# Performance work log

Hardware: AMD Instinct MI355X
Metric: run time of the kernel (lower is better)

## Reference

```python
import jax, jax.numpy as jnp
import numpy as np

PATCH = (4, 4, 4)
EMBED_DIM = 768
MASK_RATIO = 0.75
LN_EPS = 1e-3  # keras LayerNormalization default epsilon


def _sin_pos_enc_3d(nH, nW, nD, embed_dim):
    # Mirrors SinPosEncoding3D: per-axis sin/cos interleaved, concat, truncate.
    channels = int(np.ceil(embed_dim / 6) * 2)
    if channels % 2:
        channels += 1
    inv_freq = jnp.asarray(
        1.0 / np.power(10000, np.arange(0, channels, 2) / np.float32(channels)),
        dtype=jnp.float32)

    def emb1(n):
        s = jnp.arange(n, dtype=jnp.float32)[:, None] * inv_freq[None, :]  # [n, channels//2]
        return jnp.stack([jnp.sin(s), jnp.cos(s)], axis=-1).reshape(n, channels)

    ex = jnp.broadcast_to(emb1(nH)[:, None, None, :], (nH, nW, nD, channels))
    ey = jnp.broadcast_to(emb1(nW)[None, :, None, :], (nH, nW, nD, channels))
    ez = jnp.broadcast_to(emb1(nD)[None, None, :, :], (nH, nW, nD, channels))
    emb = jnp.concatenate([ex, ey, ez], axis=-1)[..., :embed_dim]
    return emb.reshape(1, nH * nW * nD, embed_dim)  # [1, token_num, E]


def setup_inputs() -> dict:
    key = jax.random.key(0)
    k1, k2, k3, k4 = jax.random.split(key, 4)
    B, H, W, D, C = 4, 96, 96, 96, 1
    nH, nW, nD = H // PATCH[0], W // PATCH[1], D // PATCH[2]
    token_num = nH * nW * nD
    mask_num = int(token_num * MASK_RATIO)
    patch_dim = PATCH[0] * PATCH[1] * PATCH[2] * C
    return {
        "x": jax.random.normal(k1, (B, H, W, D, C), dtype=jnp.float32),
        "proj_w": jax.random.normal(k2, (patch_dim, EMBED_DIM), dtype=jnp.float32) * 0.02,
        "proj_b": jnp.zeros((EMBED_DIM,), dtype=jnp.float32),
        "mask_token": jax.random.normal(k3, (1, mask_num, patch_dim), dtype=jnp.float32),
        "gamma": jnp.ones((EMBED_DIM,), dtype=jnp.float32),
        "beta": jnp.zeros((EMBED_DIM,), dtype=jnp.float32),
        "perm": jax.random.permutation(k4, token_num).astype(jnp.int32),
    }


def reference(x, proj_w, proj_b, mask_token, gamma, beta, perm):
    B, H, W, D, C = x.shape
    p0, p1, p2 = PATCH
    nH, nW, nD = H // p0, W // p1, D // p2
    token_num = nH * nW * nD
    mask_num = int(token_num * MASK_RATIO)

    # im2col-style 3D patch extraction (matches tf.extract_volume_patches layout)
    patches = x.reshape(B, nH, p0, nW, p1, nD, p2, C)
    patches = patches.transpose(0, 1, 3, 5, 2, 4, 6, 7)
    patches_flat = patches.reshape(B, token_num, p0 * p1 * p2 * C)

    mask_idx = perm[:mask_num]
    unmask_idx = perm[mask_num:]

    penc = _sin_pos_enc_3d(nH, nW, nD, EMBED_DIM)  # [1, token_num, E]

    # unmasked tokens: gather -> dense proj -> pos-enc add
    unmask_tokens = jnp.take(patches_flat, unmask_idx, axis=1)       # [B, U, pdim]
    a = jnp.einsum('bup,pe->bue', unmask_tokens, proj_w) + proj_b \
        + jnp.take(penc, unmask_idx, axis=1)                          # [B, U, E]

    # masked tokens: learned mask token -> proj -> pos-enc add, broadcast over B
    b = jnp.einsum('omp,pe->ome', mask_token, proj_w) + proj_b \
        + jnp.take(penc, mask_idx, axis=1)                            # [1, M, E]
    b = jnp.broadcast_to(b, (B, mask_num, EMBED_DIM))

    out = jnp.concatenate([a, b], axis=1).reshape(B, nH, nW, nD, EMBED_DIM)

    # LayerNorm over last axis (keras default: eps=1e-3)
    mean = jnp.mean(out, axis=-1, keepdims=True)
    var = jnp.var(out, axis=-1, keepdims=True)
    out = (out - mean) * jax.lax.rsqrt(var + LN_EPS) * gamma + beta
    return out, mask_idx
```

## Files before the change

kernel.cpp:

```cpp
#include <hip/hip_runtime.h>
#include <math.h>

#define NTHREADS 256
#define TROWS 16
#define TOKN 13824
#define MASKN 10368
#define UNMASKN 3456
#define EMB 768
#define NPOS 24
#define NBATCH 4
#define ABLOCKS (TOKN / TROWS)
#define BBLOCKS (MASKN / TROWS)
#define TABN (NPOS * 256)

__global__ __launch_bounds__(NTHREADS) void setup_kernel(
    const int* __restrict__ perm, float* __restrict__ tabg,
    float* __restrict__ out_idx)
{
  int i = blockIdx.x * NTHREADS + threadIdx.x;
  if (i < MASKN) out_idx[i] = (float)perm[i];
  if (i < TABN) {
    const float c0 = 13.287712379549449f / 128.0f;
    int pos = i >> 8, e = i & 255, j = e >> 1;
    float s = (float)pos * exp2f(-(float)j * c0);
    tabg[i] = (e & 1) ? cosf(s) : sinf(s);
  }
}

__global__ __launch_bounds__(NTHREADS) void fused_embed_ln(
    const float* __restrict__ x, const float* __restrict__ W,
    const float* __restrict__ pb, const float* __restrict__ mt,
    const float* __restrict__ gmm, const float* __restrict__ bta,
    const int* __restrict__ perm, const float* __restrict__ tabg,
    float* __restrict__ out)
{
  __shared__ __align__(16) float patch[TROWS * 64];
  __shared__ float wred[TROWS][4][2];
  __shared__ float rowstat[TROWS][2];
  __shared__ int h256[TROWS], w256[TROWS], d256[TROWS];

  const int tid = threadIdx.x;
  const int blk = blockIdx.x;
  const bool isA = blk < ABLOCKS;

  if (tid < TROWS) {
    int r;
    if (isA) {
      int row0 = blk * TROWS;
      int u = row0 % UNMASKN + tid;
      r = perm[MASKN + u];
    } else {
      int m0 = (blk - ABLOCKS) * TROWS;
      r = perm[m0 + tid];
    }
    int h = r / 576; int rem = r - h * 576;
    int w = rem / 24; int d = rem - w * 24;
    h256[tid] = h << 8; w256[tid] = w << 8; d256[tid] = d << 8;
  }
  __syncthreads();

  if (isA) {
    int b = (blk * TROWS) / UNMASKN;
    int t = tid >> 4, seg = tid & 15;
    int h = h256[t] >> 8, w = w256[t] >> 8, d = d256[t] >> 8;
    int ph = seg >> 2, pw = seg & 3;
    const float4* src = (const float4*)(x +
        ((((long)b * 96 + h * 4 + ph) * 96 + (w * 4 + pw)) * 96 + d * 4));
    ((float4*)patch)[tid] = *src;
  } else {
    int m0 = (blk - ABLOCKS) * TROWS;
    const float4* src = (const float4*)(mt + (long)m0 * 64);
    ((float4*)patch)[tid] = src[tid];
  }
  __syncthreads();

  float a0[TROWS], a1[TROWS], a2[TROWS];
  #pragma unroll
  for (int t = 0; t < TROWS; ++t) { a0[t] = 0.f; a1[t] = 0.f; a2[t] = 0.f; }

  for (int k4 = 0; k4 < 16; ++k4) {
    const float* wp = W + k4 * 4 * EMB + tid;
    float w00 = wp[0],       w01 = wp[256],         w02 = wp[512];
    float w10 = wp[EMB],     w11 = wp[EMB + 256],   w12 = wp[EMB + 512];
    float w20 = wp[2*EMB],   w21 = wp[2*EMB + 256], w22 = wp[2*EMB + 512];
    float w30 = wp[3*EMB],   w31 = wp[3*EMB + 256], w32 = wp[3*EMB + 512];
    #pragma unroll
    for (int t = 0; t < TROWS; ++t) {
      float4 p = *((const float4*)(patch + t * 64 + k4 * 4));
      a0[t] += p.x * w00; a1[t] += p.x * w01; a2[t] += p.x * w02;
      a0[t] += p.y * w10; a1[t] += p.y * w11; a2[t] += p.y * w12;
      a0[t] += p.z * w20; a1[t] += p.z * w21; a2[t] += p.z * w22;
      a0[t] += p.w * w30; a1[t] += p.w * w31; a2[t] += p.w * w32;
    }
  }

  const float pb0 = pb[tid], pb1 = pb[tid + 256], pb2 = pb[tid + 512];
  const float g0 = gmm[tid], g1 = gmm[tid + 256], g2 = gmm[tid + 512];
  const float b0 = bta[tid], b1 = bta[tid + 256], b2 = bta[tid + 512];
  const int wv = tid >> 6, ln = tid & 63;

  #pragma unroll
  for (int t = 0; t < TROWS; ++t) {
    float v0 = a0[t] + pb0 + tabg[h256[t] + tid];
    float v1 = a1[t] + pb1 + tabg[w256[t] + tid];
    float v2 = a2[t] + pb2 + tabg[d256[t] + tid];
    a0[t] = v0; a1[t] = v1; a2[t] = v2;
    float s = v0 + v1 + v2;
    float q = v0 * v0 + v1 * v1 + v2 * v2;
    #pragma unroll
    for (int off = 32; off > 0; off >>= 1) {
      s += __shfl_down(s, off, 64);
      q += __shfl_down(q, off, 64);
    }
    if (ln == 0) { wred[t][wv][0] = s; wred[t][wv][1] = q; }
  }
  __syncthreads();
  if (tid < TROWS) {
    float s = wred[tid][0][0] + wred[tid][1][0] + wred[tid][2][0] + wred[tid][3][0];
    float q = wred[tid][0][1] + wred[tid][1][1] + wred[tid][2][1] + wred[tid][3][1];
    float mean = s * (1.0f / 768.0f);
    float var = q * (1.0f / 768.0f) - mean * mean;
    rowstat[tid][0] = mean;
    rowstat[tid][1] = 1.0f / sqrtf(var + 0.001f);
  }
  __syncthreads();

  if (isA) {
    int row0 = blk * TROWS;
    int b = row0 / UNMASKN;
    int u0 = row0 % UNMASKN;
    float* base = out + ((long)b * TOKN + u0) * EMB + tid;
    #pragma unroll
    for (int t = 0; t < TROWS; ++t) {
      float mean = rowstat[t][0], rstd = rowstat[t][1];
      float* o = base + (long)t * EMB;
      o[0]   = (a0[t] - mean) * rstd * g0 + b0;
      o[256] = (a1[t] - mean) * rstd * g1 + b1;
      o[512] = (a2[t] - mean) * rstd * g2 + b2;
    }
  } else {
    int m0 = (blk - ABLOCKS) * TROWS;
    float* base = out + ((long)UNMASKN + m0) * EMB + tid;
    #pragma unroll
    for (int t = 0; t < TROWS; ++t) {
      float mean = rowstat[t][0], rstd = rowstat[t][1];
      float o0 = (a0[t] - mean) * rstd * g0 + b0;
      float o1 = (a1[t] - mean) * rstd * g1 + b1;
      float o2 = (a2[t] - mean) * rstd * g2 + b2;
      float* o = base + (long)t * EMB;
      #pragma unroll
      for (int bb = 0; bb < NBATCH; ++bb) {
        o[0] = o0; o[256] = o1; o[512] = o2;
        o += (long)TOKN * EMB;
      }
    }
  }
}

extern "C" void kernel_launch(void* const* d_in, const int* in_sizes, int n_in,
                              void* d_out, int out_size, void* d_ws, size_t ws_size,
                              hipStream_t stream) {
  const float* x    = (const float*)d_in[0];
  const float* W    = (const float*)d_in[1];
  const float* pb   = (const float*)d_in[2];
  const float* mt   = (const float*)d_in[3];
  const float* gmm  = (const float*)d_in[4];
  const float* bta  = (const float*)d_in[5];
  const int*   perm = (const int*)d_in[6];
  float* out = (float*)d_out;
  float* out_idx = out + (long)NBATCH * TOKN * EMB;
  float* tabg = (float*)d_ws;

  setup_kernel<<<(MASKN + NTHREADS - 1) / NTHREADS, NTHREADS, 0, stream>>>(
      perm, tabg, out_idx);
  fused_embed_ln<<<ABLOCKS + BBLOCKS, NTHREADS, 0, stream>>>(
      x, W, pb, mt, gmm, bta, perm, tabg, out);
}
```

Baseline: 250.0 us.

## Use bf16 MFMA for patch projection with pre-transposed bf16 weights

The fp32 FMA patch-projection loop is replaced with bf16 MFMA 16x16x32 instructions. Patches are converted to bf16 in LDS, and the setup kernel now also transposes and converts the projection weights into a bf16 workspace buffer. The LayerNorm reduction and output layout are reworked to match the MFMA accumulator layout. This lowers the compute cost of the GEMM, but bf16 inputs reduce accuracy, and the output stores now write 16-wide column chunks per row instead of full contiguous rows.

```diff
diff --git a/kernel.cpp b/kernel.cpp
--- a/kernel.cpp
+++ b/kernel.cpp
@@ -12,9 +12,20 @@
 #define ABLOCKS (TOKN / TROWS)
 #define BBLOCKS (MASKN / TROWS)
 #define TABN (NPOS * 256)
+#define WN (64 * EMB)
+
+typedef __attribute__((ext_vector_type(8))) short short8;
+typedef __attribute__((ext_vector_type(4))) float f32x4;
+
+__device__ __forceinline__ short f2bf(float f) {
+  union { float f; unsigned u; } c; c.f = f;
+  unsigned u = c.u + 0x7FFFu + ((c.u >> 16) & 1u);
+  return (short)(u >> 16);
+}
 
 __global__ __launch_bounds__(NTHREADS) void setup_kernel(
-    const int* __restrict__ perm, float* __restrict__ tabg,
+    const float* __restrict__ W, const int* __restrict__ perm,
+    float* __restrict__ tabg, short* __restrict__ wsW,
     float* __restrict__ out_idx)
 {
   int i = blockIdx.x * NTHREADS + threadIdx.x;
@@ -25,19 +36,23 @@
     float s = (float)pos * exp2f(-(float)j * c0);
     tabg[i] = (e & 1) ? cosf(s) : sinf(s);
   }
-}
-
-__global__ __launch_bounds__(NTHREADS) void fused_embed_ln(
-    const float* __restrict__ x, const float* __restrict__ W,
-    const float* __restrict__ pb, const float* __restrict__ mt,
-    const float* __restrict__ gmm, const float* __restrict__ bta,
-    const int* __restrict__ perm, const float* __restrict__ tabg,
+  if (i < WN) {
+    int col = i >> 6, k = i & 63;
+    wsW[i] = f2bf(W[k * EMB + col]);
+  }
+}
+
+__global__ __launch_bounds__(NTHREADS) void fused_embed_ln_mfma(
+    const float* __restrict__ x, const float* __restrict__ pb,
+    const float* __restrict__ mt, const float* __restrict__ gmm,
+    const float* __restrict__ bta, const int* __restrict__ perm,
+    const float* __restrict__ tabg, const short* __restrict__ wsW,
     float* __restrict__ out)
 {
-  __shared__ __align__(16) float patch[TROWS * 64];
+  __shared__ __align__(16) short aLds[TROWS][72];
+  __shared__ int segbase[3][TROWS];
   __shared__ float wred[TROWS][4][2];
   __shared__ float rowstat[TROWS][2];
-  __shared__ int h256[TROWS], w256[TROWS], d256[TROWS];
 
   const int tid = threadIdx.x;
   const int blk = blockIdx.x;
@@ -46,112 +61,127 @@
   if (tid < TROWS) {
     int r;
     if (isA) {
-      int row0 = blk * TROWS;
-      int u = row0 % UNMASKN + tid;
+      int u = (blk * TROWS) % UNMASKN + tid;
       r = perm[MASKN + u];
     } else {
-      int m0 = (blk - ABLOCKS) * TROWS;
-      r = perm[m0 + tid];
+      r = perm[(blk - ABLOCKS) * TROWS + tid];
     }
     int h = r / 576; int rem = r - h * 576;
     int w = rem / 24; int d = rem - w * 24;
-    h256[tid] = h << 8; w256[tid] = w << 8; d256[tid] = d << 8;
-  }
-  __syncthreads();
-
-  if (isA) {
-    int b = (blk * TROWS) / UNMASKN;
+    segbase[0][tid] = h << 8; segbase[1][tid] = w << 8; segbase[2][tid] = d << 8;
+  }
+  __syncthreads();
+
+  {
     int t = tid >> 4, seg = tid & 15;
-    int h = h256[t] >> 8, w = w256[t] >> 8, d = d256[t] >> 8;
-    int ph = seg >> 2, pw = seg & 3;
-    const float4* src = (const float4*)(x +
-        ((((long)b * 96 + h * 4 + ph) * 96 + (w * 4 + pw)) * 96 + d * 4));
-    ((float4*)patch)[tid] = *src;
-  } else {
-    int m0 = (blk - ABLOCKS) * TROWS;
-    const float4* src = (const float4*)(mt + (long)m0 * 64);
-    ((float4*)patch)[tid] = src[tid];
-  }
-  __syncthreads();
-
-  float a0[TROWS], a1[TROWS], a2[TROWS];
-  #pragma unroll
-  for (int t = 0; t < TROWS; ++t) { a0[t] = 0.f; a1[t] = 0.f; a2[t] = 0.f; }
-
-  for (int k4 = 0; k4 < 16; ++k4) {
-    const float* wp = W + k4 * 4 * EMB + tid;
-    float w00 = wp[0],       w01 = wp[256],         w02 = wp[512];
-    float w10 = wp[EMB],     w11 = wp[EMB + 256],   w12 = wp[EMB + 512];
-    float w20 = wp[2*EMB],   w21 = wp[2*EMB + 256], w22 = wp[2*EMB + 512];
-    float w30 = wp[3*EMB],   w31 = wp[3*EMB + 256], w32 = wp[3*EMB + 512];
-    #pragma unroll
-    for (int t = 0; t < TROWS; ++t) {
-      float4 p = *((const float4*)(patch + t * 64 + k4 * 4));
-      a0[t] += p.x * w00; a1[t] += p.x * w01; a2[t] += p.x * w02;
-      a0[t] += p.y * w10; a1[t] += p.y * w11; a2[t] += p.y * w12;
-      a0[t] += p.z * w20; a1[t] += p.z * w21; a2[t] += p.z * w22;
-      a0[t] += p.w * w30; a1[t] += p.w * w31; a2[t] += p.w * w32;
-    }
-  }
-
-  const float pb0 = pb[tid], pb1 = pb[tid + 256], pb2 = pb[tid + 512];
-  const float g0 = gmm[tid], g1 = gmm[tid + 256], g2 = gmm[tid + 512];
-  const float b0 = bta[tid], b1 = bta[tid + 256], b2 = bta[tid + 512];
-  const int wv = tid >> 6, ln = tid & 63;
-
-  #pragma unroll
-  for (int t = 0; t < TROWS; ++t) {
-    float v0 = a0[t] + pb0 + tabg[h256[t] + tid];
-    float v1 = a1[t] + pb1 + tabg[w256[t] + tid];
-    float v2 = a2[t] + pb2 + tabg[d256[t] + tid];
-    a0[t] = v0; a1[t] = v1; a2[t] = v2;
-    float s = v0 + v1 + v2;
-    float q = v0 * v0 + v1 * v1 + v2 * v2;
-    #pragma unroll
-    for (int off = 32; off > 0; off >>= 1) {
-      s += __shfl_down(s, off, 64);
-      q += __shfl_down(q, off, 64);
-    }
-    if (ln == 0) { wred[t][wv][0] = s; wred[t][wv][1] = q; }
+    float4 v;
+    if (isA) {
+      int b = (blk * TROWS) / UNMASKN;
+      int h = segbase[0][t] >> 8, w = segbase[1][t] >> 8, d = segbase[2][t] >> 8;
+      int ph = seg >> 2, pw = seg & 3;
+      v = *(const float4*)(x +
+          ((((long)b * 96 + h * 4 + ph) * 96 + (w * 4 + pw)) * 96 + d * 4));
+    } else {
+      int m0 = (blk - ABLOCKS) * TROWS;
+      v = *(const float4*)(mt + (long)(m0 + t) * 64 + seg * 4);
+    }
+    short4 s4; s4.x = f2bf(v.x); s4.y = f2bf(v.y); s4.z = f2bf(v.z); s4.w = f2bf(v.w);
+    *(short4*)&aLds[t][seg * 4] = s4;
+  }
+  __syncthreads();
+
+  const int wv = tid >> 6, lane = tid & 63;
+  const int n16 = lane & 15, q = lane >> 4;
+  const int colbase = wv * 192;
+
+  short8 af0 = *(const short8*)&aLds[n16][q * 8];
+  short8 af1 = *(const short8*)&aLds[n16][32 + q * 8];
+
+  f32x4 acc[12];
+  const short* wp = wsW + (colbase + n16) * 64 + q * 8;
+  #pragma unroll
+  for (int jt = 0; jt < 12; ++jt) {
+    short8 bf0 = *(const short8*)(wp + jt * 16 * 64);
+    short8 bf1 = *(const short8*)(wp + jt * 16 * 64 + 32);
+    f32x4 c = {0.f, 0.f, 0.f, 0.f};
+    c = __builtin_amdgcn_mfma_f32_16x16x32_bf16(af0, bf0, c, 0, 0, 0);
+    c = __builtin_amdgcn_mfma_f32_16x16x32_bf16(af1, bf1, c, 0, 0, 0);
+    acc[jt] = c;
+  }
+
+  float s[4] = {0.f, 0.f, 0.f, 0.f}, qq[4] = {0.f, 0.f, 0.f, 0.f};
+  #pragma unroll
+  for (int jt = 0; jt < 12; ++jt) {
+    int colb = colbase + jt * 16;
+    int seg = colb >> 8;
+    int cb = (colb & 255) + n16;
+    float pbj = pb[colb + n16];
+    #pragma unroll
+    for (int r = 0; r < 4; ++r) {
+      float v = acc[jt][r] + pbj + tabg[segbase[seg][q * 4 + r] + cb];
+      acc[jt][r] = v;
+      s[r] += v; qq[r] += v * v;
+    }
+  }
+  #pragma unroll
+  for (int r = 0; r < 4; ++r) {
+    #pragma unroll
+    for (int m = 8; m >= 1; m >>= 1) {
+      s[r]  += __shfl_xor(s[r],  m, 16);
+      qq[r] += __shfl_xor(qq[r], m, 16);
+    }
+  }
+  if (n16 == 0) {
+    #pragma unroll
+    for (int r = 0; r < 4; ++r) {
+      wred[q * 4 + r][wv][0] = s[r];
+      wred[q * 4 + r][wv][1] = qq[r];
+    }
   }
   __syncthreads();
   if (tid < TROWS) {
-    float s = wred[tid][0][0] + wred[tid][1][0] + wred[tid][2][0] + wred[tid][3][0];
-    float q = wred[tid][0][1] + wred[tid][1][1] + wred[tid][2][1] + wred[tid][3][1];
-    float mean = s * (1.0f / 768.0f);
-    float var = q * (1.0f / 768.0f) - mean * mean;
+    float ss = wred[tid][0][0] + wred[tid][1][0] + wred[tid][2][0] + wred[tid][3][0];
+    float qs = wred[tid][0][1] + wred[tid][1][1] + wred[tid][2][1] + wred[tid][3][1];
+    float mean = ss * (1.0f / 768.0f);
+    float var = qs * (1.0f / 768.0f) - mean * mean;
     rowstat[tid][0] = mean;
     rowstat[tid][1] = 1.0f / sqrtf(var + 0.001f);
   }
   __syncthreads();
+
+  float mr[4], rr[4];
+  #pragma unroll
+  for (int r = 0; r < 4; ++r) {
+    mr[r] = rowstat[q * 4 + r][0];
+    rr[r] = rowstat[q * 4 + r][1];
+  }
 
   if (isA) {
     int row0 = blk * TROWS;
     int b = row0 / UNMASKN;
     int u0 = row0 % UNMASKN;
-    float* base = out + ((long)b * TOKN + u0) * EMB + tid;
-    #pragma unroll
-    for (int t = 0; t < TROWS; ++t) {
-      float mean = rowstat[t][0], rstd = rowstat[t][1];
-      float* o = base + (long)t * EMB;
-      o[0]   = (a0[t] - mean) * rstd * g0 + b0;
-      o[256] = (a1[t] - mean) * rstd * g1 + b1;
-      o[512] = (a2[t] - mean) * rstd * g2 + b2;
+    float* base = out + ((long)b * TOKN + u0 + q * 4) * EMB + colbase + n16;
+    #pragma unroll
+    for (int jt = 0; jt < 12; ++jt) {
+      int col = colbase + jt * 16 + n16;
+      float g = gmm[col], bb = bta[col];
+      #pragma unroll
+      for (int r = 0; r < 4; ++r)
+        base[(long)r * EMB + jt * 16] = (acc[jt][r] - mr[r]) * rr[r] * g + bb;
     }
   } else {
     int m0 = (blk - ABLOCKS) * TROWS;
-    float* base = out + ((long)UNMASKN + m0) * EMB + tid;
-    #pragma unroll
-    for (int t = 0; t < TROWS; ++t) {
-      float mean = rowstat[t][0], rstd = rowstat[t][1];
-      float o0 = (a0[t] - mean) * rstd * g0 + b0;
-      float o1 = (a1[t] - mean) * rstd * g1 + b1;
-      float o2 = (a2[t] - mean) * rstd * g2 + b2;
-      float* o = base + (long)t * EMB;
+    float* base = out + ((long)UNMASKN + m0 + q * 4) * EMB + colbase + n16;
+    #pragma unroll
+    for (int jt = 0; jt < 12; ++jt) {
+      int col = colbase + jt * 16 + n16;
+      float g = gmm[col], bb = bta[col];
       #pragma unroll
-      for (int bb = 0; bb < NBATCH; ++bb) {
-        o[0] = o0; o[256] = o1; o[512] = o2;
-        o += (long)TOKN * EMB;
+      for (int r = 0; r < 4; ++r) {
+        float o = (acc[jt][r] - mr[r]) * rr[r] * g + bb;
+        float* p = base + (long)r * EMB + jt * 16;
+        #pragma unroll
+        for (int b4 = 0; b4 < NBATCH; ++b4) { *p = o; p += (long)TOKN * EMB; }
       }
     }
   }
@@ -169,10 +199,12 @@
   const int*   perm = (const int*)d_in[6];
   float* out = (float*)d_out;
   float* out_idx = out + (long)NBATCH * TOKN * EMB;
+
   float* tabg = (float*)d_ws;
-
-  setup_kernel<<<(MASKN + NTHREADS - 1) / NTHREADS, NTHREADS, 0, stream>>>(
-      perm, tabg, out_idx);
-  fused_embed_ln<<<ABLOCKS + BBLOCKS, NTHREADS, 0, stream>>>(
-      x, W, pb, mt, gmm, bta, perm, tabg, out);
-}
+  short* wsW  = (short*)((char*)d_ws + TABN * 4);
+
+  setup_kernel<<<(WN + NTHREADS - 1) / NTHREADS, NTHREADS, 0, stream>>>(
+      W, perm, tabg, wsW, out_idx);
+  fused_embed_ln_mfma<<<ABLOCKS + BBLOCKS, NTHREADS, 0, stream>>>(
+      x, pb, mt, gmm, bta, perm, tabg, wsW, out);
+}
```

After: 214.2 us. 14.3% less time.
